# Kernel tuning notes

Hardware: AMD Instinct MI355X
Metric: run time of the kernel (lower is better)

The kernel has to match this reference:

```python
import jax, jax.numpy as jnp
from jax import lax
import numpy as np

NUM_TOKENS = 14
DIM = 512
B, T = 32, 512


def _lstm(xs, W_ih, W_hh, b_ih, b_hh):
    """PyTorch-semantics single-layer LSTM, batch_first. xs: [B,T,D] -> hs: [B,T,D].
    Gate order i, f, g, o; gates = x @ W_ih^T + b_ih + h @ W_hh^T + b_hh."""
    Bsz, Tlen, D = xs.shape
    # Precompute input contribution for all timesteps (one big GEMM).
    pre = jnp.einsum('btd,gd->btg', xs, W_ih) + (b_ih + b_hh)  # [B,T,4D]

    def step(carry, p):
        h, c = carry
        gates = p + h @ W_hh.T  # [B,4D]
        i, f, g, o = jnp.split(gates, 4, axis=-1)
        i = jax.nn.sigmoid(i)
        f = jax.nn.sigmoid(f)
        g = jnp.tanh(g)
        o = jax.nn.sigmoid(o)
        c = f * c + i * g
        h = o * jnp.tanh(c)
        return (h, c), h

    h0 = jnp.zeros((Bsz, D), xs.dtype)
    (_, _), hs = lax.scan(step, (h0, h0), jnp.swapaxes(pre, 0, 1))  # time-major scan
    return jnp.swapaxes(hs, 0, 1)  # [B,T,D]


def setup_inputs() -> dict:
    key = jax.random.key(0)
    ks = jax.random.split(key, 10)
    s_emb = 1.0  # nn.Embedding default init N(0,1)
    s = 1.0 / np.sqrt(DIM)  # nn.LSTM default init U(-1/sqrt(H), 1/sqrt(H))
    u = lambda k, shape: jax.random.uniform(k, shape, jnp.float32, -s, s)
    return {
        'x': jax.random.randint(ks[0], (B, T), 0, NUM_TOKENS, dtype=jnp.int32),
        'embed': jax.random.normal(ks[1], (NUM_TOKENS, DIM), jnp.float32) * s_emb,
        'W_ih_q': u(ks[2], (4 * DIM, DIM)),
        'W_hh_q': u(ks[3], (4 * DIM, DIM)),
        'b_ih_q': u(ks[4], (4 * DIM,)),
        'b_hh_q': u(ks[5], (4 * DIM,)),
        'W_ih_k': u(ks[6], (4 * DIM, DIM)),
        'W_hh_k': u(ks[7], (4 * DIM, DIM)),
        'b_ih_k': u(ks[8], (4 * DIM,)),
        'b_hh_k': u(ks[9], (4 * DIM,)),
    }


def reference(x, embed, W_ih_q, W_hh_q, b_ih_q, b_hh_q, W_ih_k, W_hh_k, b_ih_k, b_hh_k):
    e = embed[x]  # [B,T,D] embedding lookup
    q = _lstm(e, W_ih_q, W_hh_q, b_ih_q, b_hh_q)  # [B,T,D]
    k = _lstm(e, W_ih_k, W_hh_k, b_ih_k, b_hh_k)  # [B,T,D]
    A = jnp.einsum('btd,bsd->bts', q, k)  # bmm(q, k^T) -> [B,T,T]
    return A
```

## Files before the change

### kernel.cpp

```cpp
#include <hip/hip_runtime.h>
#include <hip/hip_bf16.h>


#define TB 32
#define TT 512
#define TD 512
#define NTOK 14

typedef __attribute__((ext_vector_type(8))) short short8;
typedef __attribute__((ext_vector_type(4))) float f32x4;
typedef __attribute__((ext_vector_type(4))) unsigned int u32x4;

__device__ __forceinline__ float fsigmoid(float v) { return 1.f / (1.f + __expf(-v)); }
__device__ __forceinline__ float ftanh(float v) {
    float a = fabsf(v);
    float e = __expf(-2.f * a);
    float r = (1.f - e) / (1.f + e);
    return copysignf(r, v);
}
__device__ __forceinline__ unsigned short f2bf(float f) {
    __hip_bfloat16 h = __float2bfloat16(f);
    return __builtin_bit_cast(unsigned short, h);
}
__device__ __forceinline__ float bf2f(unsigned short u) {
    unsigned int x = ((unsigned int)u) << 16;
    return __builtin_bit_cast(float, x);
}

__device__ __forceinline__ u32x4 load16u_coh(const unsigned int* p) {
    u32x4 r;
    asm volatile("global_load_dwordx4 %0, %1, off sc0 sc1" : "=v"(r) : "v"(p));
    return r;
}
__device__ __forceinline__ void store4_coh(unsigned int* p, unsigned int v) {
    asm volatile("global_store_dword %0, %1, off sc0 sc1" :: "v"(p), "v"(v) : "memory");
}

__global__ __launch_bounds__(256) void pre_tab_kernel(
    const float* __restrict__ embed,
    const float* __restrict__ Wih_q, const float* __restrict__ bih_q, const float* __restrict__ bhh_q,
    const float* __restrict__ Wih_k, const float* __restrict__ bih_k, const float* __restrict__ bhh_k,
    float* __restrict__ pre)
{
    int idx = blockIdx.x * 256 + threadIdx.x;
    int l = idx / (NTOK * 4 * TD);
    int r = idx % (NTOK * 4 * TD);
    int tok = r / (4 * TD), j = r % (4 * TD);
    const float* Wih = l ? Wih_k : Wih_q;
    float acc = l ? (bih_k[j] + bhh_k[j]) : (bih_q[j] + bhh_q[j]);
    const float4* e4 = (const float4*)(embed + (size_t)tok * TD);
    const float4* w4 = (const float4*)(Wih + (size_t)j * TD);
    for (int t2 = 0; t2 < TD / 4; ++t2) {
        float4 e = e4[t2], w = w4[t2];
        acc += e.x * w.x + e.y * w.y + e.z * w.z + e.w * w.w;
    }
    pre[idx] = acc;
}

__global__ __launch_bounds__(256) void init_hbf(unsigned int* hbf) {
    hbf[blockIdx.x * 256 + threadIdx.x] = 0;
}

__global__ __launch_bounds__(256) void lstm_persist(
    const float* __restrict__ Whh_q, const float* __restrict__ Whh_k,
    const float* __restrict__ pre,
    const int* __restrict__ x,
    unsigned short* __restrict__ qh, unsigned short* __restrict__ ql,
    unsigned short* __restrict__ kh, unsigned short* __restrict__ kl,
    unsigned int* __restrict__ hbf)
{
    __shared__ unsigned short w_lds[64][512];
    __shared__ unsigned short h_lds[16][512];
    __shared__ float          g_lds[64][17];
    __shared__ unsigned char  x_lds[16 * TT];
    __shared__ float          pre_lds[NTOK][64];

    int wg  = blockIdx.x;
    int l   = wg >> 6;
    int g   = (wg >> 5) & 1;
    int wid = wg & 31;
    int d0  = wid << 4;
    int tid = threadIdx.x;
    int lane = tid & 63;
    int rt  = tid >> 6;

    const float* Whh = l ? Whh_k : Whh_q;
    unsigned short* hi_arr = l ? kh : qh;
    unsigned short* lo_arr = l ? kl : ql;
    unsigned int* hb_l = hbf + (size_t)l * 2 * TB * TD;

    {
        int r = tid >> 2;
        const float* src = Whh + (size_t)((r >> 4) * TD + d0 + (r & 15)) * TD;
#pragma unroll
        for (int i = 0; i < 16; ++i) {
            int c = (tid & 3) + 4 * i;
            float4 a = ((const float4*)src)[c * 2];
            float4 b4 = ((const float4*)src)[c * 2 + 1];
            unsigned short* dst = &w_lds[r][(c ^ (r & 7)) * 8];
            dst[0] = f2bf(a.x); dst[1] = f2bf(a.y);
            dst[2] = f2bf(a.z); dst[3] = f2bf(a.w);
            dst[4] = f2bf(b4.x); dst[5] = f2bf(b4.y);
            dst[6] = f2bf(b4.z); dst[7] = f2bf(b4.w);
        }
    }
    for (int i = tid; i < 16 * TT; i += 256)
        x_lds[i] = (unsigned char)x[(g * 16 + (i >> 9)) * TT + (i & 511)];
    for (int i = tid; i < NTOK * 64; i += 256) {
        int tok = i >> 6, j = i & 63;
        pre_lds[tok][j] = pre[((size_t)l * NTOK + tok) * (4 * TD) + (j >> 4) * TD + d0 + (j & 15)];
    }
    __syncthreads();

    int bl = tid >> 4, dd = tid & 15;
    int bg = g * 16 + bl;
    float creg = 0.f;

    {
        int tok = x_lds[bl * TT];
        float i_ = fsigmoid(pre_lds[tok][dd]);
        float f_ = fsigmoid(pre_lds[tok][16 + dd]);
        float g_ = ftanh(pre_lds[tok][32 + dd]);
        float o_ = fsigmoid(pre_lds[tok][48 + dd]);
        creg = i_ * g_;
        float h = o_ * ftanh(creg);
        unsigned short hh = f2bf(h);
        store4_coh(hb_l + (size_t)bg * TD + d0 + dd, ((unsigned int)hh << 16) | 1u);
        size_t hoff = ((size_t)bg * TT) * TD + d0 + dd;
        hi_arr[hoff] = hh;
        lo_arr[hoff] = f2bf(h - bf2f(hh));
    }

    for (int t = 1; t < TT; ++t) {
        {
            const unsigned int e = (unsigned int)t;
            int row = tid >> 4;
            const unsigned int* hb = hb_l + (size_t)((t - 1) & 1) * TB * TD
                                          + (size_t)(g * 16 + row) * TD;
            int w2 = (tid & 15) * 2;
            const unsigned int* s0 = hb + w2 * 16 + 15;
            const unsigned int* s1 = hb + (w2 + 1) * 16 + 15;
            for (;;) {
                unsigned int v0, v1;
                asm volatile("global_load_dword %0, %2, off sc0 sc1\n\t"
                             "global_load_dword %1, %3, off sc0 sc1\n\t"
                             "s_waitcnt vmcnt(0)"
                             : "=v"(v0), "=v"(v1) : "v"(s0), "v"(s1) : "memory");
                if (__all(((v0 & 0xffffu) >= e) && ((v1 & 0xffffu) >= e))) break;
                __builtin_amdgcn_s_sleep(1);
            }
            u32x4 A0[4], B0[4];
#pragma unroll
            for (int j = 0; j < 4; ++j) {
                int m = (tid & 15) + 16 * j;
                A0[j] = load16u_coh(hb + m * 8);
                B0[j] = load16u_coh(hb + m * 8 + 4);
            }
            unsigned int st = 0xFu;
            for (;;) {
                asm volatile("s_waitcnt vmcnt(0)" ::: "memory");
                __builtin_amdgcn_sched_barrier(0);
                unsigned int ns = 0;
#pragma unroll
                for (int j = 0; j < 4; ++j) if (st & (1u << j)) {
                    unsigned int bad =
                        ((A0[j].x ^ e) | (A0[j].y ^ e) | (A0[j].z ^ e) | (A0[j].w ^ e) |
                         (B0[j].x ^ e) | (B0[j].y ^ e) | (B0[j].z ^ e) | (B0[j].w ^ e)) & 0xffffu;
                    if (bad) ns |= 1u << j;
                }
                st = ns;
                if (!__any(st != 0)) break;
#pragma unroll
                for (int j = 0; j < 4; ++j) if (st & (1u << j)) {
                    int m = (tid & 15) + 16 * j;
                    A0[j] = load16u_coh(hb + m * 8);
                    B0[j] = load16u_coh(hb + m * 8 + 4);
                }
                __builtin_amdgcn_s_sleep(1);
            }
#pragma unroll
            for (int j = 0; j < 4; ++j) {
                int m = (tid & 15) + 16 * j;
                u32x4 o;
                o.x = (A0[j].x >> 16) | (A0[j].y & 0xffff0000u);
                o.y = (A0[j].z >> 16) | (A0[j].w & 0xffff0000u);
                o.z = (B0[j].x >> 16) | (B0[j].y & 0xffff0000u);
                o.w = (B0[j].z >> 16) | (B0[j].w & 0xffff0000u);
                *(u32x4*)&h_lds[row][(m ^ (row & 7)) * 8] = o;
            }
        }
        __syncthreads();

        {
            f32x4 acc = {0.f, 0.f, 0.f, 0.f};
            int rr = rt * 16 + (lane & 15);
            int hr = lane & 15;
#pragma unroll
            for (int kk = 0; kk < 16; ++kk) {
                int c = kk * 4 + (lane >> 4);
                short8 a  = *(const short8*)&h_lds[hr][(c ^ (hr & 7)) * 8];
                short8 bf = *(const short8*)&w_lds[rr][(c ^ (rr & 7)) * 8];
                acc = __builtin_amdgcn_mfma_f32_16x16x32_bf16(a, bf, acc, 0, 0, 0);
            }
            int gb = (lane >> 4) << 2;
#pragma unroll
            for (int r2 = 0; r2 < 4; ++r2) g_lds[rr][gb + r2] = acc[r2];
        }
        __syncthreads();

        {
            int tok = x_lds[bl * TT + t];
            float gi = g_lds[dd][bl]      + pre_lds[tok][dd];
            float gf = g_lds[16 + dd][bl] + pre_lds[tok][16 + dd];
            float gg = g_lds[32 + dd][bl] + pre_lds[tok][32 + dd];
            float go = g_lds[48 + dd][bl] + pre_lds[tok][48 + dd];
            float i_ = fsigmoid(gi), f_ = fsigmoid(gf), g2 = ftanh(gg), o_ = fsigmoid(go);
            creg = f_ * creg + i_ * g2;
            float h = o_ * ftanh(creg);
            unsigned short hh = f2bf(h);
            store4_coh(hb_l + (size_t)(t & 1) * TB * TD + (size_t)bg * TD + d0 + dd,
                       ((unsigned int)hh << 16) | (unsigned int)(t + 1));
            size_t hoff = ((size_t)bg * TT + t) * TD + d0 + dd;
            hi_arr[hoff] = hh;
            lo_arr[hoff] = f2bf(h - bf2f(hh));
        }
    }
}

__global__ __launch_bounds__(256) void qk_mfma(
    const unsigned short* __restrict__ qh, const unsigned short* __restrict__ ql,
    const unsigned short* __restrict__ kh, const unsigned short* __restrict__ kl,
    float* __restrict__ A)
{
    __shared__ unsigned short qh_t[64][64];
    __shared__ unsigned short ql_t[64][64];
    __shared__ unsigned short kh_t[64][64];
    __shared__ unsigned short kl_t[64][64];

    int b  = blockIdx.y;
    int t0 = (blockIdx.x >> 3) * 64;
    int s0 = (blockIdx.x & 7) * 64;
    int tid = threadIdx.x;
    int lane = tid & 63;
    int w = tid >> 6;

    int tq = w * 16 + (lane & 15);
    f32x4 acc0 = {0,0,0,0}, acc1 = {0,0,0,0}, acc2 = {0,0,0,0}, acc3 = {0,0,0,0};

    for (int kc = 0; kc < 8; ++kc) {
        for (int i = tid; i < 512; i += 256) {
            int row = i >> 3, c = i & 7;
            size_t qoff = ((size_t)b * TT + t0 + row) * TD + kc * 64 + c * 8;
            size_t koff = ((size_t)b * TT + s0 + row) * TD + kc * 64 + c * 8;
            int d = (c ^ (row & 7)) * 8;
            *(short8*)&qh_t[row][d] = *(const short8*)(qh + qoff);
            *(short8*)&ql_t[row][d] = *(const short8*)(ql + qoff);
            *(short8*)&kh_t[row][d] = *(const short8*)(kh + koff);
            *(short8*)&kl_t[row][d] = *(const short8*)(kl + koff);
        }
        __syncthreads();
#pragma unroll
        for (int kk = 0; kk < 2; ++kk) {
            int c = kk * 4 + (lane >> 4);
            short8 ah = *(const short8*)&qh_t[tq][(c ^ (tq & 7)) * 8];
            short8 al = *(const short8*)&ql_t[tq][(c ^ (tq & 7)) * 8];
#pragma unroll
            for (int st = 0; st < 4; ++st) {
                int sr = st * 16 + (lane & 15);
                short8 bh = *(const short8*)&kh_t[sr][(c ^ (sr & 7)) * 8];
                short8 bl = *(const short8*)&kl_t[sr][(c ^ (sr & 7)) * 8];
                f32x4* acc = (st == 0) ? &acc0 : (st == 1) ? &acc1 : (st == 2) ? &acc2 : &acc3;
                *acc = __builtin_amdgcn_mfma_f32_16x16x32_bf16(ah, bh, *acc, 0, 0, 0);
                *acc = __builtin_amdgcn_mfma_f32_16x16x32_bf16(ah, bl, *acc, 0, 0, 0);
                *acc = __builtin_amdgcn_mfma_f32_16x16x32_bf16(al, bh, *acc, 0, 0, 0);
            }
        }
        __syncthreads();
    }
    int m = (lane >> 4) << 2;
    size_t base = (size_t)b * TT * TT + (size_t)(t0 + w * 16 + m) * TT + s0 + (lane & 15);
#pragma unroll
    for (int r2 = 0; r2 < 4; ++r2) {
        A[base + (size_t)r2 * TT +  0] = acc0[r2];
        A[base + (size_t)r2 * TT + 16] = acc1[r2];
        A[base + (size_t)r2 * TT + 32] = acc2[r2];
        A[base + (size_t)r2 * TT + 48] = acc3[r2];
    }
}

extern "C" void kernel_launch(void* const* d_in, const int* in_sizes, int n_in,
                              void* d_out, int out_size, void* d_ws, size_t ws_size,
                              hipStream_t stream)
{
    const int*   x      = (const int*)d_in[0];
    const float* embed  = (const float*)d_in[1];
    const float* Wih_q  = (const float*)d_in[2];
    const float* Whh_q  = (const float*)d_in[3];
    const float* bih_q  = (const float*)d_in[4];
    const float* bhh_q  = (const float*)d_in[5];
    const float* Wih_k  = (const float*)d_in[6];
    const float* Whh_k  = (const float*)d_in[7];
    const float* bih_k  = (const float*)d_in[8];
    const float* bhh_k  = (const float*)d_in[9];

    unsigned short* qh = (unsigned short*)d_ws;
    unsigned short* ql = qh + (size_t)TB * TT * TD;
    unsigned short* kh = ql + (size_t)TB * TT * TD;
    unsigned short* kl = kh + (size_t)TB * TT * TD;
    float* pre = (float*)(kl + (size_t)TB * TT * TD);
    unsigned int* hbf = (unsigned int*)(pre + 2 * NTOK * 4 * TD);

    init_hbf<<<256, 256, 0, stream>>>(hbf);
    pre_tab_kernel<<<224, 256, 0, stream>>>(embed, Wih_q, bih_q, bhh_q,
                                            Wih_k, bih_k, bhh_k, pre);
    lstm_persist<<<128, 256, 0, stream>>>(Whh_q, Whh_k, pre, x,
                                          qh, ql, kh, kl, hbf);
    dim3 g2(64, 32);
    qk_mfma<<<g2, 256, 0, stream>>>(qh, ql, kh, kl, (float*)d_out);
}
```

Baseline: 1.484 ms.

## Keep gate outputs in registers via shuffles and double-buffer h in LDS

```diff
diff --git a/kernel.cpp b/kernel.cpp
--- a/kernel.cpp
+++ b/kernel.cpp
@@ -70,8 +70,7 @@
     unsigned int* __restrict__ hbf)
 {
     __shared__ unsigned short w_lds[64][512];
-    __shared__ unsigned short h_lds[16][512];
-    __shared__ float          g_lds[64][17];
+    __shared__ unsigned short h_lds[2][16][512];
     __shared__ unsigned char  x_lds[16 * TT];
     __shared__ float          pre_lds[NTOK][64];
 
@@ -91,10 +90,12 @@
 
     {
         int r = tid >> 2;
-        const float* src = Whh + (size_t)((r >> 4) * TD + d0 + (r & 15)) * TD;
-#pragma unroll
-        for (int i = 0; i < 16; ++i) {
-            int c = (tid & 3) + 4 * i;
+        int rt_r = r >> 4, i = r & 15;
+        int gate = i >> 2, dl = i & 3;
+        const float* src = Whh + (size_t)(gate * TD + d0 + rt_r * 4 + dl) * TD;
+#pragma unroll
+        for (int ii = 0; ii < 16; ++ii) {
+            int c = (tid & 3) + 4 * ii;
             float4 a = ((const float4*)src)[c * 2];
             float4 b4 = ((const float4*)src)[c * 2 + 1];
             unsigned short* dst = &w_lds[r][(c ^ (r & 7)) * 8];
@@ -112,43 +113,37 @@
     }
     __syncthreads();
 
-    int bl = tid >> 4, dd = tid & 15;
-    int bg = g * 16 + bl;
-    float creg = 0.f;
-
-    {
-        int tok = x_lds[bl * TT];
-        float i_ = fsigmoid(pre_lds[tok][dd]);
-        float f_ = fsigmoid(pre_lds[tok][16 + dd]);
-        float g_ = ftanh(pre_lds[tok][32 + dd]);
-        float o_ = fsigmoid(pre_lds[tok][48 + dd]);
-        creg = i_ * g_;
-        float h = o_ * ftanh(creg);
-        unsigned short hh = f2bf(h);
-        store4_coh(hb_l + (size_t)bg * TD + d0 + dd, ((unsigned int)hh << 16) | 1u);
-        size_t hoff = ((size_t)bg * TT) * TD + d0 + dd;
-        hi_arr[hoff] = hh;
-        lo_arr[hoff] = f2bf(h - bf2f(hh));
+    int dl = lane & 3;
+    int dim = d0 + rt * 4 + dl;
+    float creg[4] = {0.f, 0.f, 0.f, 0.f};
+
+    if ((lane & 12) == 0) {
+#pragma unroll
+        for (int r2 = 0; r2 < 4; ++r2) {
+            int bl = ((lane >> 4) << 2) + r2;
+            int bg = g * 16 + bl;
+            int tok = x_lds[bl * TT];
+            float i_ = fsigmoid(pre_lds[tok][rt * 4 + dl]);
+            float f_ = fsigmoid(pre_lds[tok][16 + rt * 4 + dl]);
+            float g_ = ftanh(pre_lds[tok][32 + rt * 4 + dl]);
+            float o_ = fsigmoid(pre_lds[tok][48 + rt * 4 + dl]);
+            creg[r2] = i_ * g_;
+            float h = o_ * ftanh(creg[r2]);
+            unsigned short hh = f2bf(h);
+            store4_coh(hb_l + (size_t)bg * TD + dim, ((unsigned int)hh << 16) | 1u);
+            size_t hoff = ((size_t)bg * TT) * TD + dim;
+            hi_arr[hoff] = hh;
+            lo_arr[hoff] = f2bf(h - bf2f(hh));
+        }
     }
 
     for (int t = 1; t < TT; ++t) {
+        int buf = (t - 1) & 1;
         {
             const unsigned int e = (unsigned int)t;
             int row = tid >> 4;
-            const unsigned int* hb = hb_l + (size_t)((t - 1) & 1) * TB * TD
+            const unsigned int* hb = hb_l + (size_t)buf * TB * TD
                                           + (size_t)(g * 16 + row) * TD;
-            int w2 = (tid & 15) * 2;
-            const unsigned int* s0 = hb + w2 * 16 + 15;
-            const unsigned int* s1 = hb + (w2 + 1) * 16 + 15;
-            for (;;) {
-                unsigned int v0, v1;
-                asm volatile("global_load_dword %0, %2, off sc0 sc1\n\t"
-                             "global_load_dword %1, %3, off sc0 sc1\n\t"
-                             "s_waitcnt vmcnt(0)"
-                             : "=v"(v0), "=v"(v1) : "v"(s0), "v"(s1) : "memory");
-                if (__all(((v0 & 0xffffu) >= e) && ((v1 & 0xffffu) >= e))) break;
-                __builtin_amdgcn_s_sleep(1);
-            }
             u32x4 A0[4], B0[4];
 #pragma unroll
             for (int j = 0; j < 4; ++j) {
@@ -156,10 +151,25 @@
                 A0[j] = load16u_coh(hb + m * 8);
                 B0[j] = load16u_coh(hb + m * 8 + 4);
             }
+            int w2 = (tid & 15) * 2;
+            const unsigned int* s0p = hb + w2 * 16 + 15;
+            const unsigned int* s1p = hb + (w2 + 1) * 16 + 15;
+            unsigned int v0, v1;
+            asm volatile("global_load_dword %0, %1, off sc0 sc1" : "=v"(v0) : "v"(s0p));
+            asm volatile("global_load_dword %0, %1, off sc0 sc1" : "=v"(v1) : "v"(s1p));
+            asm volatile("s_waitcnt vmcnt(0)" ::: "memory");
+            __builtin_amdgcn_sched_barrier(0);
+            int tries = 0;
+            for (;;) {
+                if (__all(((v0 & 0xffffu) >= e) && ((v1 & 0xffffu) >= e))) break;
+                if (++tries > 4) __builtin_amdgcn_s_sleep(1);
+                asm volatile("global_load_dword %0, %1, off sc0 sc1" : "=v"(v0) : "v"(s0p));
+                asm volatile("global_load_dword %0, %1, off sc0 sc1" : "=v"(v1) : "v"(s1p));
+                asm volatile("s_waitcnt vmcnt(0)" ::: "memory");
+                __builtin_amdgcn_sched_barrier(0);
+            }
             unsigned int st = 0xFu;
             for (;;) {
-                asm volatile("s_waitcnt vmcnt(0)" ::: "memory");
-                __builtin_amdgcn_sched_barrier(0);
                 unsigned int ns = 0;
 #pragma unroll
                 for (int j = 0; j < 4; ++j) if (st & (1u << j)) {
@@ -176,7 +186,8 @@
                     A0[j] = load16u_coh(hb + m * 8);
                     B0[j] = load16u_coh(hb + m * 8 + 4);
                 }
-                __builtin_amdgcn_s_sleep(1);
+                asm volatile("s_waitcnt vmcnt(0)" ::: "memory");
+                __builtin_amdgcn_sched_barrier(0);
             }
 #pragma unroll
             for (int j = 0; j < 4; ++j) {
@@ -186,43 +197,51 @@
                 o.y = (A0[j].z >> 16) | (A0[j].w & 0xffff0000u);
                 o.z = (B0[j].x >> 16) | (B0[j].y & 0xffff0000u);
                 o.w = (B0[j].z >> 16) | (B0[j].w & 0xffff0000u);
-                *(u32x4*)&h_lds[row][(m ^ (row & 7)) * 8] = o;
+                *(u32x4*)&h_lds[buf][row][(m ^ (row & 7)) * 8] = o;
             }
         }
         __syncthreads();
 
+        f32x4 acc = {0.f, 0.f, 0.f, 0.f};
         {
-            f32x4 acc = {0.f, 0.f, 0.f, 0.f};
             int rr = rt * 16 + (lane & 15);
             int hr = lane & 15;
 #pragma unroll
             for (int kk = 0; kk < 16; ++kk) {
                 int c = kk * 4 + (lane >> 4);
-                short8 a  = *(const short8*)&h_lds[hr][(c ^ (hr & 7)) * 8];
+                short8 a  = *(const short8*)&h_lds[buf][hr][(c ^ (hr & 7)) * 8];
                 short8 bf = *(const short8*)&w_lds[rr][(c ^ (rr & 7)) * 8];
                 acc = __builtin_amdgcn_mfma_f32_16x16x32_bf16(a, bf, acc, 0, 0, 0);
             }
-            int gb = (lane >> 4) << 2;
-#pragma unroll
-            for (int r2 = 0; r2 < 4; ++r2) g_lds[rr][gb + r2] = acc[r2];
-        }
-        __syncthreads();
-
-        {
-            int tok = x_lds[bl * TT + t];
-            float gi = g_lds[dd][bl]      + pre_lds[tok][dd];
-            float gf = g_lds[16 + dd][bl] + pre_lds[tok][16 + dd];
-            float gg = g_lds[32 + dd][bl] + pre_lds[tok][32 + dd];
-            float go = g_lds[48 + dd][bl] + pre_lds[tok][48 + dd];
-            float i_ = fsigmoid(gi), f_ = fsigmoid(gf), g2 = ftanh(gg), o_ = fsigmoid(go);
-            creg = f_ * creg + i_ * g2;
-            float h = o_ * ftanh(creg);
-            unsigned short hh = f2bf(h);
-            store4_coh(hb_l + (size_t)(t & 1) * TB * TD + (size_t)bg * TD + d0 + dd,
-                       ((unsigned int)hh << 16) | (unsigned int)(t + 1));
-            size_t hoff = ((size_t)bg * TT + t) * TD + d0 + dd;
-            hi_arr[hoff] = hh;
-            lo_arr[hoff] = f2bf(h - bf2f(hh));
+        }
+
+        float gfv[4], ggv[4], gov[4];
+#pragma unroll
+        for (int r2 = 0; r2 < 4; ++r2) {
+            gfv[r2] = __shfl_xor(acc[r2], 4);
+            ggv[r2] = __shfl_xor(acc[r2], 8);
+            gov[r2] = __shfl_xor(acc[r2], 12);
+        }
+        if ((lane & 12) == 0) {
+#pragma unroll
+            for (int r2 = 0; r2 < 4; ++r2) {
+                int bl = ((lane >> 4) << 2) + r2;
+                int bg = g * 16 + bl;
+                int tok = x_lds[bl * TT + t];
+                float gi = acc[r2] + pre_lds[tok][rt * 4 + dl];
+                float gf = gfv[r2] + pre_lds[tok][16 + rt * 4 + dl];
+                float gg = ggv[r2] + pre_lds[tok][32 + rt * 4 + dl];
+                float go = gov[r2] + pre_lds[tok][48 + rt * 4 + dl];
+                float i_ = fsigmoid(gi), f_ = fsigmoid(gf), g2 = ftanh(gg), o_ = fsigmoid(go);
+                creg[r2] = f_ * creg[r2] + i_ * g2;
+                float h = o_ * ftanh(creg[r2]);
+                unsigned short hh = f2bf(h);
+                store4_coh(hb_l + (size_t)(t & 1) * TB * TD + (size_t)bg * TD + dim,
+                           ((unsigned int)hh << 16) | (unsigned int)(t + 1));
+                size_t hoff = ((size_t)bg * TT + t) * TD + dim;
+                hi_arr[hoff] = hh;
+                lo_arr[hoff] = f2bf(h - bf2f(hh));
+            }
         }
     }
 }
```

Result: slower. 2.161 ms (+45.6%).
